# Performance work log

Measured on AMD Instinct MI355X. Metric: run time of the kernel, lower is better.

## Reference

```python
import jax, jax.numpy as jnp
import numpy as np

N = 100_000      # nodes
E = 3_200_000    # edges (avg degree 32)
F_IN = 128       # num_features
DIM = 10         # hidden dim (module default)
B = 1000         # graphs in the batch


def setup_inputs() -> dict:
    key = jax.random.key(0)
    k1, k2, k3, k4, k5, k6 = jax.random.split(key, 6)
    x = jax.random.normal(k1, (N, F_IN), dtype=jnp.float32)
    edge_index = jax.random.randint(k2, (2, E), 0, N)
    batch = jnp.sort(jax.random.randint(k3, (N,), 0, B))
    # SAGEConv with concat=True has weight shape [2*in, out], no bias
    W1 = jax.random.normal(k4, (2 * F_IN, DIM), dtype=jnp.float32) * 0.05
    W2 = jax.random.normal(k5, (2 * DIM, DIM), dtype=jnp.float32) * 0.1
    Wfc = jax.random.normal(k6, (DIM, 1), dtype=jnp.float32) * 0.1
    return {"x": x, "edge_index": edge_index, "batch": batch,
            "W1": W1, "W2": W2, "Wfc": Wfc}


def _segment_mean(vals, idx, num_segments):
    s = jax.ops.segment_sum(vals, idx, num_segments=num_segments)
    c = jax.ops.segment_sum(jnp.ones((vals.shape[0],), vals.dtype), idx,
                            num_segments=num_segments)
    return s / jnp.maximum(c, 1.0)[:, None]


def _sage_conv(x, src, dst, W):
    # message = x[src]; mean-aggregate into dst; cat([x, aggr]) @ W
    aggr = _segment_mean(x[src], dst, N)          # [N, F]
    return jnp.concatenate([x, aggr], axis=-1) @ W  # [N, out]


def reference(x, edge_index, batch, W1, W2, Wfc):
    src, dst = edge_index[0], edge_index[1]
    h = jax.nn.relu(_sage_conv(x, src, dst, W1))   # [N, DIM]
    h = _sage_conv(h, src, dst, W2)                # [N, DIM]
    g = _segment_mean(h, batch, B)                 # [B, DIM] global_mean_pool
    return jax.nn.sigmoid(g @ Wfc)                 # [B, 1]
```

## Files before the change

kernel.cpp:

```cpp
#include <hip/hip_runtime.h>
#include <cstdint>

typedef unsigned int u32;
typedef unsigned short u16;

#define N_NODES 100000
#define N_EDGES 3200000
#define F_IN 128
#define DIM 10
#define QB 16
#define B_GRAPHS 1000
#define FRONT_T 512
#define NBLK_N 196

#define SHIFTC 7
#define NBINS 128
#define NCB 782
#define CAPC 4608
#define CHUNK_C 8192
#define NBLK_C 391
#define SEGW 129
#define TW (NCB + 1)

__device__ __forceinline__ u16 f2b(float f) {
  union { float f; u32 i; } c; c.f = f;
  u32 r = c.i + 0x7FFFu + ((c.i >> 16) & 1u);
  return (u16)(r >> 16);
}
__device__ __forceinline__ float bl(u32 u) {
  union { u32 i; float f; } c; c.i = u << 16; return c.f;
}
__device__ __forceinline__ float bh(u32 u) {
  union { u32 i; float f; } c; c.i = u & 0xFFFF0000u; return c.f;
}

__device__ __forceinline__ void gemm_body(
    int bid, int tid,
    const float* __restrict__ x, const float* __restrict__ W,
    float* __restrict__ p1, u16* __restrict__ q1b)
{
  int i = bid * FRONT_T + tid;
  if (i >= N_NODES) return;
  const float4* __restrict__ xr = (const float4*)(x + (size_t)i * F_IN);
  float ap[DIM], aq[DIM];
  #pragma unroll
  for (int j = 0; j < DIM; ++j) { ap[j] = 0.f; aq[j] = 0.f; }
  #pragma unroll 4
  for (int k4 = 0; k4 < F_IN / 4; ++k4) {
    float4 v = xr[k4];
    const float* __restrict__ w0 = W + (k4 * 4) * DIM;
    const float* __restrict__ w1 = W + (F_IN + k4 * 4) * DIM;
    #pragma unroll
    for (int j = 0; j < DIM; ++j) {
      ap[j] += v.x * w0[j] + v.y * w0[DIM + j] + v.z * w0[2 * DIM + j] + v.w * w0[3 * DIM + j];
      aq[j] += v.x * w1[j] + v.y * w1[DIM + j] + v.z * w1[2 * DIM + j] + v.w * w1[3 * DIM + j];
    }
  }
  float* pr = p1 + (size_t)i * DIM;
  #pragma unroll
  for (int j = 0; j < DIM; ++j) pr[j] = ap[j];
  u32* qr = (u32*)(q1b + (size_t)i * QB);
  uint4 v0; u32 v1;
  v0.x = (u32)f2b(aq[0]) | ((u32)f2b(aq[1]) << 16);
  v0.y = (u32)f2b(aq[2]) | ((u32)f2b(aq[3]) << 16);
  v0.z = (u32)f2b(aq[4]) | ((u32)f2b(aq[5]) << 16);
  v0.w = (u32)f2b(aq[6]) | ((u32)f2b(aq[7]) << 16);
  v1   = (u32)f2b(aq[8]) | ((u32)f2b(aq[9]) << 16);
  *(uint4*)qr = v0;
  qr[4] = v1;
}

__device__ __forceinline__ void coarse_body(
    int bid, int tid,
    const int* __restrict__ src, const int* __restrict__ dst,
    u32* __restrict__ rec, u32* __restrict__ segt)
{
  __shared__ u32 srt[CHUNK_C];
  __shared__ u32 segst[NCB + 1];
  __shared__ u32 rank[NCB];
  __shared__ u32 wtot[4];

  for (int t = tid; t < NCB; t += FRONT_T) rank[t] = 0u;
  __syncthreads();

  int base = bid * CHUNK_C;
  const int4* __restrict__ dst4 = (const int4*)dst;
  const int4* __restrict__ src4 = (const int4*)src;
  #pragma unroll
  for (int it = 0; it < CHUNK_C / (FRONT_T * 4); ++it) {
    int e = base + it * (FRONT_T * 4) + tid * 4;
    if (e < N_EDGES) {
      int4 d = dst4[(base >> 2) + it * FRONT_T + tid];
      atomicAdd(&rank[(u32)d.x >> SHIFTC], 1u);
      atomicAdd(&rank[(u32)d.y >> SHIFTC], 1u);
      atomicAdd(&rank[(u32)d.z >> SHIFTC], 1u);
      atomicAdd(&rank[(u32)d.w >> SHIFTC], 1u);
    }
  }
  __syncthreads();

  if (tid < 256) {
    u32 lh[4] = {0u, 0u, 0u, 0u};
    u32 lsum = 0u;
    if (tid < 196) {
      #pragma unroll
      for (int k = 0; k < 4; ++k) {
        int b4 = tid * 4 + k;
        lh[k] = (b4 < NCB) ? rank[b4] : 0u;
        lsum += lh[k];
      }
    }
    u32 v = lsum;
    #pragma unroll
    for (int off = 1; off < 64; off <<= 1) {
      u32 t = __shfl_up(v, off, 64);
      if ((tid & 63) >= off) v += t;
    }
    if ((tid & 63) == 63) wtot[tid >> 6] = v;
    __syncthreads();
    u32 wofs = 0u;
    #pragma unroll
    for (int w = 0; w < 3; ++w) if ((tid >> 6) > w) wofs += wtot[w];
    if (tid < 196) {
      u32 excl = wofs + v - lsum;
      #pragma unroll
      for (int k = 0; k < 4; ++k) {
        int b4 = tid * 4 + k;
        if (b4 < NCB) segst[b4] = excl;
        excl += lh[k];
      }
      if (tid == 195) segst[NCB] = excl;
    }
  } else {
    __syncthreads();
  }
  __syncthreads();

  for (int t = tid; t < NCB; t += FRONT_T) rank[t] = 0u;
  __syncthreads();

  #pragma unroll
  for (int it = 0; it < CHUNK_C / (FRONT_T * 4); ++it) {
    int e = base + it * (FRONT_T * 4) + tid * 4;
    if (e < N_EDGES) {
      int4 d = dst4[(base >> 2) + it * FRONT_T + tid];
      int4 s = src4[(base >> 2) + it * FRONT_T + tid];
      #pragma unroll
      for (int q = 0; q < 4; ++q) {
        u32 dd = (u32)((q == 0) ? d.x : (q == 1) ? d.y : (q == 2) ? d.z : d.w);
        u32 ss = (u32)((q == 0) ? s.x : (q == 1) ? s.y : (q == 2) ? s.z : s.w);
        u32 cb = dd >> SHIFTC;
        u32 pos = segst[cb] + atomicAdd(&rank[cb], 1u);
        srt[pos] = ((dd & (NBINS - 1u)) << 17) | ss;
      }
    }
  }
  __syncthreads();

  for (int k = tid; k <= NCB; k += FRONT_T)
    segt[(size_t)bid * TW + k] = segst[k];
  int total = (int)segst[NCB];
  for (int t = tid; t < total; t += FRONT_T)
    rec[base + t] = srt[t];
}

__global__ __launch_bounds__(FRONT_T) void k_front(
    const int* __restrict__ src, const int* __restrict__ dst,
    u32* __restrict__ rec, u32* __restrict__ segt,
    const float* __restrict__ x, const float* __restrict__ W,
    float* __restrict__ p1, u16* __restrict__ q1b)
{
  if (blockIdx.x < NBLK_C)
    coarse_body(blockIdx.x, threadIdx.x, src, dst, rec, segt);
  else
    gemm_body(blockIdx.x - NBLK_C, threadIdx.x, x, W, p1, q1b);
}

#define SEG_GATHER(QSRC)                                                      \
  float s[DIM];                                                               \
  _Pragma("unroll")                                                           \
  for (int j = 0; j < DIM; ++j) s[j] = 0.f;                                   \
  {                                                                           \
    int k = st + l;                                                           \
    for (; k + 8 < en; k += 16) {                                             \
      int s0 = (int)srt[k], s1 = (int)srt[k + 8];                             \
      const u32* __restrict__ q0 = (const u32*)(QSRC + (size_t)s0 * QB);      \
      const u32* __restrict__ q1 = (const u32*)(QSRC + (size_t)s1 * QB);      \
      uint4 A0 = *(const uint4*)q0; u32 B0 = q0[4];                           \
      uint4 A1 = *(const uint4*)q1; u32 B1 = q1[4];                           \
      s[0] += bl(A0.x) + bl(A1.x); s[1] += bh(A0.x) + bh(A1.x);               \
      s[2] += bl(A0.y) + bl(A1.y); s[3] += bh(A0.y) + bh(A1.y);               \
      s[4] += bl(A0.z) + bl(A1.z); s[5] += bh(A0.z) + bh(A1.z);               \
      s[6] += bl(A0.w) + bl(A1.w); s[7] += bh(A0.w) + bh(A1.w);               \
      s[8] += bl(B0) + bl(B1);     s[9] += bh(B0) + bh(B1);                   \
    }                                                                         \
    if (k < en) {                                                             \
      int s0 = (int)srt[k];                                                   \
      const u32* __restrict__ q0 = (const u32*)(QSRC + (size_t)s0 * QB);      \
      uint4 A0 = *(const uint4*)q0; u32 B0 = q0[4];                           \
      s[0] += bl(A0.x); s[1] += bh(A0.x);                                     \
      s[2] += bl(A0.y); s[3] += bh(A0.y);                                     \
      s[4] += bl(A0.z); s[5] += bh(A0.z);                                     \
      s[6] += bl(A0.w); s[7] += bh(A0.w);                                     \
      s[8] += bl(B0);   s[9] += bh(B0);                                       \
    }                                                                         \
  }                                                                           \
  _Pragma("unroll")                                                           \
  for (int m = 1; m < 8; m <<= 1) {                                           \
    _Pragma("unroll")                                                         \
    for (int j = 0; j < DIM; ++j) s[j] += __shfl_xor(s[j], m, 8);             \
  }

__global__ __launch_bounds__(512) void k_lay1(
    const u32* __restrict__ rec, const u32* __restrict__ segt,
    const float* __restrict__ p1, const u16* __restrict__ q1b,
    const float* __restrict__ W2, const float* __restrict__ Wfc,
    float* __restrict__ y, float* __restrict__ z,
    u32* __restrict__ sortrec, u32* __restrict__ segg)
{
  __shared__ u32 lrec[CAPC];
  __shared__ u32 srt[CAPC];
  __shared__ u32 hist[NBINS];
  __shared__ u32 segst[NBINS + 1];
  __shared__ u32 rank[NBINS];
  __shared__ u32 wtot[2];
  __shared__ u32 bst[NBLK_C];
  __shared__ u32 ntot_s;
  __shared__ float wv[2 * DIM];
  int tid = threadIdx.x;
  int c = blockIdx.x;
  if (tid < 2 * DIM) {
    float sacc = 0.f;
    #pragma unroll
    for (int j = 0; j < DIM; ++j) sacc += W2[tid * DIM + j] * Wfc[j];
    wv[tid] = sacc;
  }
  if (tid < NBINS) { hist[tid] = 0u; rank[tid] = 0u; }
  u32 cnt = 0u;
  if (tid < NBLK_C)
    cnt = segt[(size_t)tid * TW + c + 1] - segt[(size_t)tid * TW + c];
  srt[tid] = cnt;
  __syncthreads();
  for (int off = 1; off < 512; off <<= 1) {
    u32 v = (tid >= off) ? srt[tid - off] : 0u;
    __syncthreads();
    if (tid >= off) srt[tid] += v;
    __syncthreads();
  }
  if (tid < NBLK_C) bst[tid] = srt[tid] - cnt;
  if (tid == NBLK_C - 1) ntot_s = srt[tid];
  __syncthreads();
  int n = min((int)ntot_s, CAPC);
  {
    int grp = tid >> 3, l = tid & 7;
    for (int b = grp; b < NBLK_C; b += 64) {
      u32 s0 = segt[(size_t)b * TW + c];
      u32 cn = segt[(size_t)b * TW + c + 1] - s0;
      const u32* __restrict__ rp = rec + (size_t)b * CHUNK_C + s0;
      u32 bb = bst[b];
      for (u32 r = l; r < cn; r += 8u) {
        u32 pos = bb + r;
        if (pos < (u32)CAPC) {
          u32 v = rp[r];
          lrec[pos] = v;
          atomicAdd(&hist[(v >> 17) & (NBINS - 1u)], 1u);
        }
      }
    }
  }
  __syncthreads();
  if (tid < NBINS) {
    u32 h = hist[tid];
    u32 v = h;
    #pragma unroll
    for (int off = 1; off < 64; off <<= 1) {
      u32 t = __shfl_up(v, off, 64);
      if ((tid & 63) >= off) v += t;
    }
    if ((tid & 63) == 63) wtot[tid >> 6] = v;
    segst[tid] = v - h;
  }
  __syncthreads();
  if (tid >= 64 && tid < NBINS) segst[tid] += wtot[0];
  if (tid == 0) segst[NBINS] = wtot[0] + wtot[1];
  __syncthreads();
  for (int r = tid; r < n; r += 512) {
    u32 v = lrec[r];
    u32 dl = (v >> 17) & (NBINS - 1u);
    u32 pos = segst[dl] + atomicAdd(&rank[dl], 1u);
    srt[pos] = v & 0x1FFFFu;
  }
  __syncthreads();
  for (int r = tid; r < n; r += 512) sortrec[(size_t)c * CAPC + r] = srt[r];
  if (tid <= NBINS) segg[(size_t)c * SEGW + tid] = segst[tid];
  int g0 = tid >> 3, l = tid & 7;
  #pragma unroll
  for (int rd = 0; rd < 2; ++rd) {
    int g2 = rd * 64 + g0;
    int st = (int)segst[g2], en = (int)segst[g2 + 1];
    SEG_GATHER(q1b)
    if (l == 0) {
      int i = c * NBINS + g2;
      if (i < N_NODES) {
        float dinv = 1.0f / fmaxf((float)(en - st), 1.0f);
        const float* __restrict__ pr = p1 + (size_t)i * DIM;
        float yv = 0.f, zv = 0.f;
        #pragma unroll
        for (int j = 0; j < DIM; ++j) {
          float h = fmaxf(pr[j] + s[j] * dinv, 0.0f);
          yv += h * wv[j];
          zv += h * wv[DIM + j];
        }
        y[i] = yv;
        z[i] = zv;
      }
    }
  }
}

__global__ __launch_bounds__(256) void k_zpool(
    const u32* __restrict__ sortrec, const u32* __restrict__ segg,
    const float* __restrict__ y, const float* __restrict__ z,
    const int* __restrict__ batch, float* __restrict__ out)
{
  __shared__ float wsum[4];
  int g = blockIdx.x;
  int tid = threadIdx.x;
  int lo = 0, hi = N_NODES;
  while (lo < hi) { int m = (lo + hi) >> 1; if (batch[m] < g) lo = m + 1; else hi = m; }
  int start = lo;
  hi = N_NODES;
  while (lo < hi) { int m = (lo + hi) >> 1; if (batch[m] < g + 1) lo = m + 1; else hi = m; }
  int end = lo;
  int grp = tid >> 3, l = tid & 7;
  float acc = 0.f;
  for (int i = start + grp; i < end; i += 32) {
    int c = i >> SHIFTC, bin = i & (NBINS - 1);
    u32 st = segg[(size_t)c * SEGW + bin];
    u32 en = segg[(size_t)c * SEGW + bin + 1];
    const u32* __restrict__ rc = sortrec + (size_t)c * CAPC;
    float sc = 0.f;
    for (u32 k = st + l; k < en; k += 8u) sc += z[rc[k]];
    #pragma unroll
    for (int m = 1; m < 8; m <<= 1) sc += __shfl_xor(sc, m, 8);
    if (l == 0) acc += y[i] + sc / fmaxf((float)(en - st), 1.0f);
  }
  if (l != 0) acc = 0.f;
  #pragma unroll
  for (int m = 1; m < 64; m <<= 1) acc += __shfl_xor(acc, m, 64);
  if ((tid & 63) == 0) wsum[tid >> 6] = acc;
  __syncthreads();
  if (tid == 0) {
    float tot = wsum[0] + wsum[1] + wsum[2] + wsum[3];
    float gm = tot / fmaxf((float)(end - start), 1.0f);
    out[g] = 1.0f / (1.0f + expf(-gm));
  }
}

extern "C" void kernel_launch(void* const* d_in, const int* in_sizes, int n_in,
                              void* d_out, int out_size, void* d_ws, size_t ws_size,
                              hipStream_t stream)
{
  const float* x     = (const float*)d_in[0];
  const int*   ei    = (const int*)d_in[1];
  const int*   batch = (const int*)d_in[2];
  const float* W1    = (const float*)d_in[3];
  const float* W2    = (const float*)d_in[4];
  const float* Wfc   = (const float*)d_in[5];
  float* out = (float*)d_out;

  const int* src = ei;
  const int* dst = ei + N_EDGES;

  u32* wsp = (u32*)d_ws;
  u32* rec     = wsp;
  u32* segt    = rec + (size_t)NBLK_C * CHUNK_C;
  u32* sortrec = segt + 306176;
  u32* segg    = sortrec + (size_t)NCB * CAPC;
  u32* after   = segg + 100928;
  u16*   q1b = (u16*)after;
  float* p1  = (float*)(after + 800000);
  float* y   = (float*)(after + 1800000);
  float* z   = (float*)(after + 1900096);

  k_front<<<NBLK_C + NBLK_N, FRONT_T, 0, stream>>>(src, dst, rec, segt,
                                                   x, W1, p1, q1b);
  k_lay1<<<NCB, 512, 0, stream>>>(rec, segt, p1, q1b, W2, Wfc, y, z,
                                  sortrec, segg);
  k_zpool<<<B_GRAPHS, 256, 0, stream>>>(sortrec, segg, y, z, batch, out);
}
```

Measured before the change: 185.6 us.

## Drop LDS record staging buffer; re-read records from global in scatter pass

Removes the lrec shared buffer and instead reads each record from global memory twice: once for the histogram and once for the bucket scatter. The per-chunk offset scan is rewritten from a 512-thread, 9-step LDS Hillis-Steele scan with many barriers into a 4-per-thread local sum plus a wavefront shuffle scan. This cuts LDS usage, which may allow more blocks per CU, and removes barriers, at the cost of an extra global (likely L2-resident) read of the records. The overflow check also moves from the staging position to the sorted position.

```diff
diff --git a/kernel.cpp b/kernel.cpp
--- a/kernel.cpp
+++ b/kernel.cpp
@@ -218,12 +218,12 @@
     float* __restrict__ y, float* __restrict__ z,
     u32* __restrict__ sortrec, u32* __restrict__ segg)
 {
-  __shared__ u32 lrec[CAPC];
   __shared__ u32 srt[CAPC];
   __shared__ u32 hist[NBINS];
   __shared__ u32 segst[NBINS + 1];
   __shared__ u32 rank[NBINS];
   __shared__ u32 wtot[2];
+  __shared__ u32 cwtot[4];
   __shared__ u32 bst[NBLK_C];
   __shared__ u32 ntot_s;
   __shared__ float wv[2 * DIM];
@@ -236,37 +236,53 @@
     wv[tid] = sacc;
   }
   if (tid < NBINS) { hist[tid] = 0u; rank[tid] = 0u; }
-  u32 cnt = 0u;
-  if (tid < NBLK_C)
-    cnt = segt[(size_t)tid * TW + c + 1] - segt[(size_t)tid * TW + c];
-  srt[tid] = cnt;
-  __syncthreads();
-  for (int off = 1; off < 512; off <<= 1) {
-    u32 v = (tid >= off) ? srt[tid - off] : 0u;
+
+  if (tid < 256) {
+    u32 lh[4] = {0u, 0u, 0u, 0u};
+    u32 lsum = 0u;
+    if (tid < 98) {
+      #pragma unroll
+      for (int k = 0; k < 4; ++k) {
+        int b4 = tid * 4 + k;
+        if (b4 < NBLK_C) {
+          lh[k] = segt[(size_t)b4 * TW + c + 1] - segt[(size_t)b4 * TW + c];
+          lsum += lh[k];
+        }
+      }
+    }
+    u32 v = lsum;
+    #pragma unroll
+    for (int off = 1; off < 64; off <<= 1) {
+      u32 t = __shfl_up(v, off, 64);
+      if ((tid & 63) >= off) v += t;
+    }
+    if ((tid & 63) == 63) cwtot[tid >> 6] = v;
     __syncthreads();
-    if (tid >= off) srt[tid] += v;
+    u32 wofs = 0u;
+    #pragma unroll
+    for (int w = 0; w < 3; ++w) if ((tid >> 6) > w) wofs += cwtot[w];
+    if (tid < 98) {
+      u32 excl = wofs + v - lsum;
+      #pragma unroll
+      for (int k = 0; k < 4; ++k) {
+        int b4 = tid * 4 + k;
+        if (b4 < NBLK_C) { bst[b4] = excl; excl += lh[k]; }
+      }
+      if (tid == 97) ntot_s = excl;
+    }
+  } else {
     __syncthreads();
   }
-  if (tid < NBLK_C) bst[tid] = srt[tid] - cnt;
-  if (tid == NBLK_C - 1) ntot_s = srt[tid];
   __syncthreads();
   int n = min((int)ntot_s, CAPC);
-  {
-    int grp = tid >> 3, l = tid & 7;
-    for (int b = grp; b < NBLK_C; b += 64) {
-      u32 s0 = segt[(size_t)b * TW + c];
-      u32 cn = segt[(size_t)b * TW + c + 1] - s0;
-      const u32* __restrict__ rp = rec + (size_t)b * CHUNK_C + s0;
-      u32 bb = bst[b];
-      for (u32 r = l; r < cn; r += 8u) {
-        u32 pos = bb + r;
-        if (pos < (u32)CAPC) {
-          u32 v = rp[r];
-          lrec[pos] = v;
-          atomicAdd(&hist[(v >> 17) & (NBINS - 1u)], 1u);
-        }
-      }
-    }
+  int grp = tid >> 3, l = tid & 7;
+
+  for (int b = grp; b < NBLK_C; b += 64) {
+    u32 s0 = segt[(size_t)b * TW + c];
+    u32 cn = segt[(size_t)b * TW + c + 1] - s0;
+    const u32* __restrict__ rp = rec + (size_t)b * CHUNK_C + s0;
+    for (u32 r = l; r < cn; r += 8u)
+      atomicAdd(&hist[(rp[r] >> 17) & (NBINS - 1u)], 1u);
   }
   __syncthreads();
   if (tid < NBINS) {
@@ -284,16 +300,22 @@
   if (tid >= 64 && tid < NBINS) segst[tid] += wtot[0];
   if (tid == 0) segst[NBINS] = wtot[0] + wtot[1];
   __syncthreads();
-  for (int r = tid; r < n; r += 512) {
-    u32 v = lrec[r];
-    u32 dl = (v >> 17) & (NBINS - 1u);
-    u32 pos = segst[dl] + atomicAdd(&rank[dl], 1u);
-    srt[pos] = v & 0x1FFFFu;
+  for (int b = grp; b < NBLK_C; b += 64) {
+    u32 s0 = segt[(size_t)b * TW + c];
+    u32 cn = segt[(size_t)b * TW + c + 1] - s0;
+    const u32* __restrict__ rp = rec + (size_t)b * CHUNK_C + s0;
+    for (u32 r = l; r < cn; r += 8u) {
+      u32 v = rp[r];
+      u32 dl = (v >> 17) & (NBINS - 1u);
+      u32 pos = segst[dl] + atomicAdd(&rank[dl], 1u);
+      if (pos < (u32)CAPC)
+        srt[pos] = v & 0x1FFFFu;
+    }
   }
   __syncthreads();
   for (int r = tid; r < n; r += 512) sortrec[(size_t)c * CAPC + r] = srt[r];
   if (tid <= NBINS) segg[(size_t)c * SEGW + tid] = segst[tid];
-  int g0 = tid >> 3, l = tid & 7;
+  int g0 = grp;
   #pragma unroll
   for (int rd = 0; rd < 2; ++rd) {
     int g2 = rd * 64 + g0;
```

New measurement: 194.0 us. 1.05x slower.
